# Kernel optimization log

Measured on AMD Instinct MI355X. Metric: run time of the kernel, lower is better.

## Reference

```python
import jax, jax.numpy as jnp
import numpy as np

T, B, H, D = 512, 64, 512, 32  # timesteps, batch, hidden_size, process_dim


def _softplus_beta(x, beta):
    # torch.nn.Softplus(beta): log(1+exp(beta*x))/beta
    return jax.nn.softplus(beta * x) / beta


def setup_inputs() -> dict:
    key = jax.random.key(0)
    ks = jax.random.split(key, 5)
    seq_dt = jax.random.uniform(ks[0], (T, B), jnp.float32)  # time until next event
    seq_types = jax.random.randint(ks[1], (T, B), 0, D)      # event type ids in [0, D)
    embed = jax.random.normal(ks[2], (D + 1, D), jnp.float32) * 0.1
    embed = embed.at[D].set(0.0)  # padding_idx row
    # 7 gate linears fused: order [input_g, forget_g, output_g, input_target, forget_target, z_gate, decay]
    W_gates = jax.random.normal(ks[3], (D + H, 7 * H), jnp.float32) * (1.0 / np.sqrt(D + H))
    b_gates = jax.random.normal(ks[4], (7 * H,), jnp.float32) * 0.05
    h0 = jnp.zeros((B, H), jnp.float32)
    c0 = jnp.zeros((B, H), jnp.float32)
    c_target0 = jnp.zeros((B, H), jnp.float32)
    return dict(seq_dt=seq_dt, seq_types=seq_types, embed=embed,
                W_gates=W_gates, b_gates=b_gates, h0=h0, c0=c0, c_target0=c_target0)


def reference(seq_dt, seq_types, embed, W_gates, b_gates, h0, c0, c_target0):
    def step(carry, inp):
        h, c, ctar = carry
        dt, types = inp
        x = embed[types]                       # (B, D) event embedding
        v = jnp.concatenate([x, h], axis=1)    # (B, D+H)
        g = v @ W_gates + b_gates              # (B, 7H) fused gate GEMM
        gi, gf, go, git, gft, gz, gd = jnp.split(g, 7, axis=1)
        inpt = jax.nn.sigmoid(gi)
        forget = jax.nn.sigmoid(gf)
        output = jax.nn.sigmoid(go)
        in_tar = jax.nn.sigmoid(git)
        fg_tar = jax.nn.sigmoid(gft)
        z = jnp.tanh(gz)
        decay = _softplus_beta(gd, 10.0)
        c_i = forget * c + inpt * z
        ctar_new = fg_tar * ctar + in_tar * z
        c_t = ctar_new + (c_i - ctar_new) * jnp.exp(-decay * dt[:, None])
        h_t = output * jnp.tanh(c_t)
        return (h_t, c_t, ctar_new), (h_t, output, c_i, ctar_new, decay)

    _, outs = jax.lax.scan(step, (h0, c0, c_target0), (seq_dt, seq_types))
    # (hiddens_ti, outputs, cells, cell_targets, decays), each (T, B, H)
    return outs
```

## Files before the change

### kernel.cpp

```cpp
#include <hip/hip_runtime.h>
#include <math.h>

#define T_ 512
#define B_ 64
#define H_ 512
#define D_ 32
#define G7H (7*H_)
#define NBLK 128
#define NTHR 256
#define JPB 4
#define BH (B_*H_)

typedef _Float16 f16x8 __attribute__((ext_vector_type(8)));
typedef float f32x4  __attribute__((ext_vector_type(4)));
typedef int   i32x2  __attribute__((ext_vector_type(2)));

__global__ void precompute_P2(const float* __restrict__ embed,
                              const float* __restrict__ Wg,
                              const float* __restrict__ bg,
                              float* __restrict__ P2) {
    int idx = blockIdx.x * blockDim.x + threadIdx.x;
    if (idx >= 33 * H_ * 8) return;
    int gate = idx & 7;
    int j    = (idx >> 3) & (H_ - 1);
    int type = idx >> 12;
    float acc = 0.f;
    if (gate < 7) {
        acc = bg[gate * H_ + j];
        #pragma unroll
        for (int d = 0; d < D_; ++d)
            acc += embed[type * D_ + d] * Wg[(size_t)d * G7H + gate * H_ + j];
    }
    P2[idx] = acc;
}

__global__ void precompute_Wt16(const float* __restrict__ Wg,
                                _Float16* __restrict__ Wt) {
    int idx = blockIdx.x * blockDim.x + threadIdx.x;
    if (idx >= G7H * H_) return;
    int k = idx & (H_ - 1);
    int n = idx >> 9;
    Wt[idx] = (_Float16)Wg[(size_t)(D_ + k) * G7H + n];
}

__global__ void init_h16(const float* __restrict__ h0, _Float16* __restrict__ hf) {
    int idx = blockIdx.x * blockDim.x + threadIdx.x;
    if (idx >= BH) return;
    hf[idx] = (_Float16)h0[idx];
}

__device__ __forceinline__ float fast_rcp(float x) {
    float r;
    asm("v_rcp_f32 %0, %1" : "=v"(r) : "v"(x));
    return r;
}
__device__ __forceinline__ float fast_sigmoid(float x) {
    return fast_rcp(1.f + __expf(-x));
}
__device__ __forceinline__ float fast_tanh(float x) {
    return 1.f - 2.f * fast_rcp(1.f + __expf(2.f * x));
}

#define LOADA(dst, p, OFF) \
    asm volatile("global_load_dwordx4 %0, %1, off offset:" #OFF " sc1" \
                 : "=v"(dst) : "v"(p) : "memory")

__global__ void __launch_bounds__(NTHR, 1)
hawkes_main(const float* __restrict__ seq_dt, const int* __restrict__ seq_types,
            const float* __restrict__ c0, const float* __restrict__ ct0,
            const float* __restrict__ P2,
            const _Float16* __restrict__ Wt,
            _Float16* __restrict__ hf,
            int* __restrict__ flags,
            float* __restrict__ out) {
    __shared__ float gl[B_][36];

    const int tid  = threadIdx.x;
    const int w    = tid >> 6;
    const int lane = tid & 63;
    const int bid  = blockIdx.x;
    const int j0   = (bid & 7) * 64 + (bid >> 3) * JPB;
    const int m0   = w * 16;
    const int krow = (lane >> 4) << 3;

    f16x8 Bf[2][16];
    {
        const f16x8 zf = {0, 0, 0, 0, 0, 0, 0, 0};
        #pragma unroll
        for (int nt = 0; nt < 2; ++nt) {
            const int cl = nt * 16 + (lane & 15);
            const int gate = cl & 7, jl2 = cl >> 3;
            const bool pad = (gate == 7);
            const size_t nb = pad ? 0 : (size_t)(gate * H_ + j0 + jl2) * (size_t)H_;
            #pragma unroll
            for (int kt = 0; kt < 16; ++kt) {
                f16x8 v = *(const f16x8*)(Wt + nb + kt * 32 + krow);
                Bf[nt][kt] = pad ? zf : v;
            }
        }
    }

    const int eb = tid >> 2, ejl = tid & 3, ej = j0 + ejl;
    float c_s  = c0 [eb * H_ + ej];
    float ct_s = ct0[eb * H_ + ej];

    int   typ = seq_types[eb];
    float dtv = seq_dt[eb];
    float4 pa, pb;
    {
        const float* pr = P2 + ((size_t)typ * H_ + ej) * 8;
        pa = *(const float4*)pr;
        pb = *(const float4*)(pr + 4);
    }

    const size_t TBH = (size_t)T_ * BH;
    const int arow = m0 + (lane & 15);

    for (int t = 0; t < T_; ++t) {
        const _Float16* ph = hf + (t & 1) * BH + arow * H_ + krow;
        f16x8 Af[16];
        LOADA(Af[0],  ph, 0);    LOADA(Af[1],  ph, 64);
        LOADA(Af[2],  ph, 128);  LOADA(Af[3],  ph, 192);
        LOADA(Af[4],  ph, 256);  LOADA(Af[5],  ph, 320);
        LOADA(Af[6],  ph, 384);  LOADA(Af[7],  ph, 448);
        LOADA(Af[8],  ph, 512);  LOADA(Af[9],  ph, 576);
        LOADA(Af[10], ph, 640);  LOADA(Af[11], ph, 704);
        LOADA(Af[12], ph, 768);  LOADA(Af[13], ph, 832);
        LOADA(Af[14], ph, 896);  LOADA(Af[15], ph, 960);
        asm volatile("s_waitcnt vmcnt(0)" ::: "memory");
        __builtin_amdgcn_sched_barrier(0);

        f32x4 a0 = {0.f,0.f,0.f,0.f}, a1 = {0.f,0.f,0.f,0.f};
        #pragma unroll
        for (int kt = 0; kt < 16; ++kt) {
            a0 = __builtin_amdgcn_mfma_f32_16x16x32_f16(Af[kt], Bf[0][kt], a0, 0, 0, 0);
            a1 = __builtin_amdgcn_mfma_f32_16x16x32_f16(Af[kt], Bf[1][kt], a1, 0, 0, 0);
        }

        {
            const int col = lane & 15, rbase = m0 + ((lane >> 4) << 2);
            #pragma unroll
            for (int r = 0; r < 4; ++r) {
                gl[rbase + r][col]      = a0[r];
                gl[rbase + r][16 + col] = a1[r];
            }
        }
        asm volatile("s_waitcnt lgkmcnt(0)" ::: "memory");
        __builtin_amdgcn_sched_barrier(0);

        float4 ga = *(const float4*)&gl[eb][ejl * 8];
        float4 gb = *(const float4*)&gl[eb][ejl * 8 + 4];
        const float g0 = ga.x + pa.x, g1 = ga.y + pa.y, g2 = ga.z + pa.z, g3 = ga.w + pa.w;
        const float g4 = gb.x + pb.x, g5 = gb.y + pb.y, g6 = gb.z + pb.z;

        const float inpt   = fast_sigmoid(g0);
        const float forget = fast_sigmoid(g1);
        const float outp   = fast_sigmoid(g2);
        const float in_tar = fast_sigmoid(g3);
        const float fg_tar = fast_sigmoid(g4);
        const float z      = fast_tanh(g5);
        const float y      = 10.f * g6;
        const float decay  = (fmaxf(y, 0.f) + __logf(1.f + __expf(-fabsf(y)))) * 0.1f;

        const float c_i      = forget * c_s + inpt * z;
        const float ctar_new = fg_tar * ct_s + in_tar * z;
        const float c_t = ctar_new + (c_i - ctar_new) * __expf(-decay * dtv);
        const float h_t = outp * fast_tanh(c_t);
        c_s  = c_t;
        ct_s = ctar_new;

        {
            union { _Float16 f; unsigned short u; } cv; cv.f = (_Float16)h_t;
            unsigned hs = cv.u;
            unsigned oh = (unsigned)__shfl_down((int)hs, 1);
            if ((ejl & 1) == 0) {
                unsigned* dh = (unsigned*)(hf + ((t + 1) & 1) * BH) + ((eb * H_ + ej) >> 1);
                __hip_atomic_store(dh, hs | (oh << 16), __ATOMIC_RELAXED, __HIP_MEMORY_SCOPE_AGENT);
            }
        }

        __syncthreads();
        if (tid == 0)
            __hip_atomic_store(flags + bid, t + 1, __ATOMIC_RELAXED, __HIP_MEMORY_SCOPE_AGENT);

        {
            const size_t base = (size_t)t * BH + (size_t)eb * H_ + ej;
            out[base]           = h_t;
            out[TBH + base]     = outp;
            out[2 * TBH + base] = c_i;
            out[3 * TBH + base] = ctar_new;
            out[4 * TBH + base] = decay;
        }

        {
            const int tn = (t + 1 < T_) ? t + 1 : t;
            typ = seq_types[tn * B_ + eb];
            dtv = seq_dt  [tn * B_ + eb];
            const float* pr = P2 + ((size_t)typ * H_ + ej) * 8;
            pa = *(const float4*)pr;
            pb = *(const float4*)(pr + 4);
        }

        if (t + 1 < T_) {
            if (w == 0) {
                const int* fp = flags + 2 * lane;
                int ok;
                do {
                    i32x2 vv;
                    asm volatile("global_load_dwordx2 %0, %1, off sc1\n\t"
                                 "s_waitcnt vmcnt(0)"
                                 : "=&v"(vv) : "v"(fp) : "memory");
                    ok = (vv.x >= t + 1) && (vv.y >= t + 1);
                } while (!__all(ok));
            }
            __syncthreads();
        }
    }
}

extern "C" void kernel_launch(void* const* d_in, const int* in_sizes, int n_in,
                              void* d_out, int out_size, void* d_ws, size_t ws_size,
                              hipStream_t stream) {
    const float* seq_dt    = (const float*)d_in[0];
    const int*   seq_types = (const int*)  d_in[1];
    const float* embed     = (const float*)d_in[2];
    const float* W_gates   = (const float*)d_in[3];
    const float* b_gates   = (const float*)d_in[4];
    const float* h0        = (const float*)d_in[5];
    const float* c0        = (const float*)d_in[6];
    const float* ct0       = (const float*)d_in[7];
    float* out = (float*)d_out;

    float* P2 = (float*)d_ws;
    _Float16* Wt = (_Float16*)(P2 + 33 * H_ * 8);
    _Float16* hf = Wt + (size_t)G7H * H_;
    int* flags = (int*)(hf + 2 * BH);

    hipMemsetAsync(flags, 0, NBLK * sizeof(int), stream);
    {
        int total = 33 * H_ * 8;
        precompute_P2<<<(total + 255) / 256, 256, 0, stream>>>(embed, W_gates, b_gates, P2);
    }
    {
        int total = G7H * H_;
        precompute_Wt16<<<(total + 255) / 256, 256, 0, stream>>>(W_gates, Wt);
    }
    {
        int total = BH;
        init_h16<<<(total + 255) / 256, 256, 0, stream>>>(h0, hf);
    }
    {
        void* args[] = {(void*)&seq_dt, (void*)&seq_types, (void*)&c0, (void*)&ct0,
                        (void*)&P2, (void*)&Wt, (void*)&hf, (void*)&flags, (void*)&out};
        hipLaunchCooperativeKernel((void*)hawkes_main, dim3(NBLK), dim3(NTHR),
                                   args, 0, stream);
    }
}
```

Measured before the change: 1.908 ms.

## Replace per-block flag barrier with tagged h-value polling in fp16 LSB

Removes the per-step flag store, __syncthreads, and flag polling used as a grid-wide barrier. Instead it embeds a parity tag in the low mantissa bit of each fp16 h value, and each wave re-loads its A operand until every element carries the expected tag. This is meant to cut the barrier round-trip latency from the sequential recurrence, so each block waits only on the data it consumes. It also splits the MFMA accumulation chain into two accumulators. The cost is a loss of one mantissa bit of h precision, and the correctness of the scheme relies on per-dword atomic visibility.

```diff
diff --git a/kernel.cpp b/kernel.cpp
--- a/kernel.cpp
+++ b/kernel.cpp
@@ -13,7 +13,6 @@
 
 typedef _Float16 f16x8 __attribute__((ext_vector_type(8)));
 typedef float f32x4  __attribute__((ext_vector_type(4)));
-typedef int   i32x2  __attribute__((ext_vector_type(2)));
 
 __global__ void precompute_P2(const float* __restrict__ embed,
                               const float* __restrict__ Wg,
@@ -43,10 +42,15 @@
     Wt[idx] = (_Float16)Wg[(size_t)(D_ + k) * G7H + n];
 }
 
-__global__ void init_h16(const float* __restrict__ h0, _Float16* __restrict__ hf) {
+__global__ void init_h16(const float* __restrict__ h0, unsigned* __restrict__ hfu) {
     int idx = blockIdx.x * blockDim.x + threadIdx.x;
-    if (idx >= BH) return;
-    hf[idx] = (_Float16)h0[idx];
+    if (idx >= BH / 2) return;
+    union { _Float16 f; unsigned short u; } lo, hi;
+    lo.f = (_Float16)h0[2 * idx];
+    hi.f = (_Float16)h0[2 * idx + 1];
+    unsigned v = ((unsigned)(lo.u & 0xFFFEu)) | (((unsigned)(hi.u & 0xFFFEu)) << 16);
+    __hip_atomic_store(hfu + idx, v, __ATOMIC_RELAXED, __HIP_MEMORY_SCOPE_AGENT);
+    __hip_atomic_store(hfu + BH / 2 + idx, 0x00010001u, __ATOMIC_RELAXED, __HIP_MEMORY_SCOPE_AGENT);
 }
 
 __device__ __forceinline__ float fast_rcp(float x) {
@@ -64,6 +68,33 @@
 #define LOADA(dst, p, OFF) \
     asm volatile("global_load_dwordx4 %0, %1, off offset:" #OFF " sc1" \
                  : "=v"(dst) : "v"(p) : "memory")
+
+template<int RTAG>
+__device__ __forceinline__ void poll_load(f16x8 Af[16], const _Float16* ph) {
+    while (true) {
+        LOADA(Af[0],  ph, 0);    LOADA(Af[1],  ph, 64);
+        LOADA(Af[2],  ph, 128);  LOADA(Af[3],  ph, 192);
+        LOADA(Af[4],  ph, 256);  LOADA(Af[5],  ph, 320);
+        LOADA(Af[6],  ph, 384);  LOADA(Af[7],  ph, 448);
+        LOADA(Af[8],  ph, 512);  LOADA(Af[9],  ph, 576);
+        LOADA(Af[10], ph, 640);  LOADA(Af[11], ph, 704);
+        LOADA(Af[12], ph, 768);  LOADA(Af[13], ph, 832);
+        LOADA(Af[14], ph, 896);  LOADA(Af[15], ph, 960);
+        asm volatile("s_waitcnt vmcnt(0)" ::: "memory");
+        __builtin_amdgcn_sched_barrier(0);
+        unsigned acc = RTAG ? 0xFFFFFFFFu : 0u;
+        #pragma unroll
+        for (int kt = 0; kt < 16; ++kt) {
+            union { f16x8 f; unsigned u[4]; } c; c.f = Af[kt];
+            if (RTAG) acc &= c.u[0] & c.u[1] & c.u[2] & c.u[3];
+            else      acc |= c.u[0] | c.u[1] | c.u[2] | c.u[3];
+        }
+        const bool ok = RTAG ? ((acc & 0x00010001u) == 0x00010001u)
+                             : ((acc & 0x00010001u) == 0u);
+        if (__all(ok)) break;
+    }
+    __builtin_amdgcn_sched_barrier(0);
+}
 
 __global__ void __launch_bounds__(NTHR, 1)
 hawkes_main(const float* __restrict__ seq_dt, const int* __restrict__ seq_types,
@@ -71,7 +102,6 @@
             const float* __restrict__ P2,
             const _Float16* __restrict__ Wt,
             _Float16* __restrict__ hf,
-            int* __restrict__ flags,
             float* __restrict__ out) {
     __shared__ float gl[B_][36];
 
@@ -119,23 +149,19 @@
     for (int t = 0; t < T_; ++t) {
         const _Float16* ph = hf + (t & 1) * BH + arow * H_ + krow;
         f16x8 Af[16];
-        LOADA(Af[0],  ph, 0);    LOADA(Af[1],  ph, 64);
-        LOADA(Af[2],  ph, 128);  LOADA(Af[3],  ph, 192);
-        LOADA(Af[4],  ph, 256);  LOADA(Af[5],  ph, 320);
-        LOADA(Af[6],  ph, 384);  LOADA(Af[7],  ph, 448);
-        LOADA(Af[8],  ph, 512);  LOADA(Af[9],  ph, 576);
-        LOADA(Af[10], ph, 640);  LOADA(Af[11], ph, 704);
-        LOADA(Af[12], ph, 768);  LOADA(Af[13], ph, 832);
-        LOADA(Af[14], ph, 896);  LOADA(Af[15], ph, 960);
-        asm volatile("s_waitcnt vmcnt(0)" ::: "memory");
-        __builtin_amdgcn_sched_barrier(0);
-
-        f32x4 a0 = {0.f,0.f,0.f,0.f}, a1 = {0.f,0.f,0.f,0.f};
-        #pragma unroll
-        for (int kt = 0; kt < 16; ++kt) {
-            a0 = __builtin_amdgcn_mfma_f32_16x16x32_f16(Af[kt], Bf[0][kt], a0, 0, 0, 0);
-            a1 = __builtin_amdgcn_mfma_f32_16x16x32_f16(Af[kt], Bf[1][kt], a1, 0, 0, 0);
-        }
+        if ((t >> 1) & 1) poll_load<1>(Af, ph);
+        else              poll_load<0>(Af, ph);
+
+        f32x4 a0a = {0.f,0.f,0.f,0.f}, a0b = {0.f,0.f,0.f,0.f};
+        f32x4 a1a = {0.f,0.f,0.f,0.f}, a1b = {0.f,0.f,0.f,0.f};
+        #pragma unroll
+        for (int kt = 0; kt < 16; kt += 2) {
+            a0a = __builtin_amdgcn_mfma_f32_16x16x32_f16(Af[kt],     Bf[0][kt],     a0a, 0, 0, 0);
+            a1a = __builtin_amdgcn_mfma_f32_16x16x32_f16(Af[kt],     Bf[1][kt],     a1a, 0, 0, 0);
+            a0b = __builtin_amdgcn_mfma_f32_16x16x32_f16(Af[kt + 1], Bf[0][kt + 1], a0b, 0, 0, 0);
+            a1b = __builtin_amdgcn_mfma_f32_16x16x32_f16(Af[kt + 1], Bf[1][kt + 1], a1b, 0, 0, 0);
+        }
+        const f32x4 a0 = a0a + a0b, a1 = a1a + a1b;
 
         {
             const int col = lane & 15, rbase = m0 + ((lane >> 4) << 2);
@@ -170,18 +196,15 @@
         ct_s = ctar_new;
 
         {
+            const unsigned wtag = ((unsigned)(t + 1) >> 1) & 1u;
             union { _Float16 f; unsigned short u; } cv; cv.f = (_Float16)h_t;
-            unsigned hs = cv.u;
+            unsigned hs = ((unsigned)cv.u & 0xFFFEu) | wtag;
             unsigned oh = (unsigned)__shfl_down((int)hs, 1);
             if ((ejl & 1) == 0) {
                 unsigned* dh = (unsigned*)(hf + ((t + 1) & 1) * BH) + ((eb * H_ + ej) >> 1);
                 __hip_atomic_store(dh, hs | (oh << 16), __ATOMIC_RELAXED, __HIP_MEMORY_SCOPE_AGENT);
             }
         }
-
-        __syncthreads();
-        if (tid == 0)
-            __hip_atomic_store(flags + bid, t + 1, __ATOMIC_RELAXED, __HIP_MEMORY_SCOPE_AGENT);
 
         {
             const size_t base = (size_t)t * BH + (size_t)eb * H_ + ej;
@@ -199,21 +222,6 @@
             const float* pr = P2 + ((size_t)typ * H_ + ej) * 8;
             pa = *(const float4*)pr;
             pb = *(const float4*)(pr + 4);
-        }
-
-        if (t + 1 < T_) {
-            if (w == 0) {
-                const int* fp = flags + 2 * lane;
-                int ok;
-                do {
-                    i32x2 vv;
-                    asm volatile("global_load_dwordx2 %0, %1, off sc1\n\t"
-                                 "s_waitcnt vmcnt(0)"
-                                 : "=&v"(vv) : "v"(fp) : "memory");
-                    ok = (vv.x >= t + 1) && (vv.y >= t + 1);
-                } while (!__all(ok));
-            }
-            __syncthreads();
         }
     }
 }
@@ -234,9 +242,7 @@
     float* P2 = (float*)d_ws;
     _Float16* Wt = (_Float16*)(P2 + 33 * H_ * 8);
     _Float16* hf = Wt + (size_t)G7H * H_;
-    int* flags = (int*)(hf + 2 * BH);
-
-    hipMemsetAsync(flags, 0, NBLK * sizeof(int), stream);
+
     {
         int total = 33 * H_ * 8;
         precompute_P2<<<(total + 255) / 256, 256, 0, stream>>>(embed, W_gates, b_gates, P2);
@@ -246,12 +252,12 @@
         precompute_Wt16<<<(total + 255) / 256, 256, 0, stream>>>(W_gates, Wt);
     }
     {
-        int total = BH;
-        init_h16<<<(total + 255) / 256, 256, 0, stream>>>(h0, hf);
+        int total = BH / 2;
+        init_h16<<<(total + 255) / 256, 256, 0, stream>>>(h0, (unsigned*)hf);
     }
     {
         void* args[] = {(void*)&seq_dt, (void*)&seq_types, (void*)&c0, (void*)&ct0,
-                        (void*)&P2, (void*)&Wt, (void*)&hf, (void*)&flags, (void*)&out};
+                        (void*)&P2, (void*)&Wt, (void*)&hf, (void*)&out};
         hipLaunchCooperativeKernel((void*)hawkes_main, dim3(NBLK), dim3(NTHR),
                                    args, 0, stream);
     }
```

Result: slower. 3.305 ms (+73.2%).

## Replace block-level barrier with per-wave flags and overlap output stores with polling

Applied to the files above, without the earlier changes.

Each wave now publishes its own progress flag (512 flags in total) and polls all flags itself, so the two __syncthreads per step are removed. The output stores and next-step input loads are issued while the flag loads are in flight, hiding their latency behind the grid-wide wait. The MFMA reduction is also split across two accumulator chains per output tile to shorten the dependent chain. In exchange, every wave polls four times as many flags, which adds memory traffic during the spin-wait, and the flag buffer is enlarged to match.

```diff
diff --git a/kernel.cpp b/kernel.cpp
--- a/kernel.cpp
+++ b/kernel.cpp
@@ -13,7 +13,7 @@
 
 typedef _Float16 f16x8 __attribute__((ext_vector_type(8)));
 typedef float f32x4  __attribute__((ext_vector_type(4)));
-typedef int   i32x2  __attribute__((ext_vector_type(2)));
+typedef int   i32x4  __attribute__((ext_vector_type(4)));
 
 __global__ void precompute_P2(const float* __restrict__ embed,
                               const float* __restrict__ Wg,
@@ -65,6 +65,11 @@
     asm volatile("global_load_dwordx4 %0, %1, off offset:" #OFF " sc1" \
                  : "=v"(dst) : "v"(p) : "memory")
 
+#define LOADF(v0, v1, p) \
+    asm volatile("global_load_dwordx4 %0, %2, off sc1\n\t" \
+                 "global_load_dwordx4 %1, %2, off offset:16 sc1" \
+                 : "=&v"(v0), "=&v"(v1) : "v"(p) : "memory")
+
 __global__ void __launch_bounds__(NTHR, 1)
 hawkes_main(const float* __restrict__ seq_dt, const int* __restrict__ seq_types,
             const float* __restrict__ c0, const float* __restrict__ ct0,
@@ -115,6 +120,8 @@
 
     const size_t TBH = (size_t)T_ * BH;
     const int arow = m0 + (lane & 15);
+    int* const myflag = flags + w * NBLK + bid;
+    const int* const fp = flags + lane * 8;
 
     for (int t = 0; t < T_; ++t) {
         const _Float16* ph = hf + (t & 1) * BH + arow * H_ + krow;
@@ -130,12 +137,16 @@
         asm volatile("s_waitcnt vmcnt(0)" ::: "memory");
         __builtin_amdgcn_sched_barrier(0);
 
-        f32x4 a0 = {0.f,0.f,0.f,0.f}, a1 = {0.f,0.f,0.f,0.f};
+        f32x4 a0a = {0.f,0.f,0.f,0.f}, a0b = {0.f,0.f,0.f,0.f};
+        f32x4 a1a = {0.f,0.f,0.f,0.f}, a1b = {0.f,0.f,0.f,0.f};
         #pragma unroll
-        for (int kt = 0; kt < 16; ++kt) {
-            a0 = __builtin_amdgcn_mfma_f32_16x16x32_f16(Af[kt], Bf[0][kt], a0, 0, 0, 0);
-            a1 = __builtin_amdgcn_mfma_f32_16x16x32_f16(Af[kt], Bf[1][kt], a1, 0, 0, 0);
-        }
+        for (int kt = 0; kt < 16; kt += 2) {
+            a0a = __builtin_amdgcn_mfma_f32_16x16x32_f16(Af[kt],     Bf[0][kt],     a0a, 0, 0, 0);
+            a1a = __builtin_amdgcn_mfma_f32_16x16x32_f16(Af[kt],     Bf[1][kt],     a1a, 0, 0, 0);
+            a0b = __builtin_amdgcn_mfma_f32_16x16x32_f16(Af[kt + 1], Bf[0][kt + 1], a0b, 0, 0, 0);
+            a1b = __builtin_amdgcn_mfma_f32_16x16x32_f16(Af[kt + 1], Bf[1][kt + 1], a1b, 0, 0, 0);
+        }
+        const f32x4 a0 = a0a + a0b, a1 = a1a + a1b;
 
         {
             const int col = lane & 15, rbase = m0 + ((lane >> 4) << 2);
@@ -179,41 +190,46 @@
             }
         }
 
-        __syncthreads();
-        if (tid == 0)
-            __hip_atomic_store(flags + bid, t + 1, __ATOMIC_RELAXED, __HIP_MEMORY_SCOPE_AGENT);
-
-        {
+        asm volatile("s_waitcnt vmcnt(0)" ::: "memory");
+        __builtin_amdgcn_sched_barrier(0);
+        if (lane == 0)
+            __hip_atomic_store(myflag, t + 1, __ATOMIC_RELAXED, __HIP_MEMORY_SCOPE_AGENT);
+
+        if (t + 1 < T_) {
+            i32x4 v0, v1;
+            LOADF(v0, v1, fp);
+
+            {
+                const size_t base = (size_t)t * BH + (size_t)eb * H_ + ej;
+                out[base]           = h_t;
+                out[TBH + base]     = outp;
+                out[2 * TBH + base] = c_i;
+                out[3 * TBH + base] = ctar_new;
+                out[4 * TBH + base] = decay;
+            }
+            typ = seq_types[(t + 1) * B_ + eb];
+            dtv = seq_dt  [(t + 1) * B_ + eb];
+            const float* pr = P2 + ((size_t)typ * H_ + ej) * 8;
+            pa = *(const float4*)pr;
+            pb = *(const float4*)(pr + 4);
+
+            asm volatile("s_waitcnt vmcnt(0)" ::: "memory");
+            int ok = (v0.x >= t + 1) && (v0.y >= t + 1) && (v0.z >= t + 1) && (v0.w >= t + 1) &&
+                     (v1.x >= t + 1) && (v1.y >= t + 1) && (v1.z >= t + 1) && (v1.w >= t + 1);
+            while (!__all(ok)) {
+                LOADF(v0, v1, fp);
+                asm volatile("s_waitcnt vmcnt(0)" ::: "memory");
+                ok = (v0.x >= t + 1) && (v0.y >= t + 1) && (v0.z >= t + 1) && (v0.w >= t + 1) &&
+                     (v1.x >= t + 1) && (v1.y >= t + 1) && (v1.z >= t + 1) && (v1.w >= t + 1);
+            }
+            __builtin_amdgcn_sched_barrier(0);
+        } else {
             const size_t base = (size_t)t * BH + (size_t)eb * H_ + ej;
             out[base]           = h_t;
             out[TBH + base]     = outp;
             out[2 * TBH + base] = c_i;
             out[3 * TBH + base] = ctar_new;
             out[4 * TBH + base] = decay;
-        }
-
-        {
-            const int tn = (t + 1 < T_) ? t + 1 : t;
-            typ = seq_types[tn * B_ + eb];
-            dtv = seq_dt  [tn * B_ + eb];
-            const float* pr = P2 + ((size_t)typ * H_ + ej) * 8;
-            pa = *(const float4*)pr;
-            pb = *(const float4*)(pr + 4);
-        }
-
-        if (t + 1 < T_) {
-            if (w == 0) {
-                const int* fp = flags + 2 * lane;
-                int ok;
-                do {
-                    i32x2 vv;
-                    asm volatile("global_load_dwordx2 %0, %1, off sc1\n\t"
-                                 "s_waitcnt vmcnt(0)"
-                                 : "=&v"(vv) : "v"(fp) : "memory");
-                    ok = (vv.x >= t + 1) && (vv.y >= t + 1);
-                } while (!__all(ok));
-            }
-            __syncthreads();
         }
     }
 }
@@ -236,7 +252,7 @@
     _Float16* hf = Wt + (size_t)G7H * H_;
     int* flags = (int*)(hf + 2 * BH);
 
-    hipMemsetAsync(flags, 0, NBLK * sizeof(int), stream);
+    hipMemsetAsync(flags, 0, 512 * sizeof(int), stream);
     {
         int total = 33 * H_ * 8;
         precompute_P2<<<(total + 255) / 256, 256, 0, stream>>>(embed, W_gates, b_gates, P2);
```

Result: slower. 4.768 ms (+150.0%).
